# Kernel optimization log

Measured on AMD Instinct MI355X. Metric: run time of the kernel, lower is better.

Reference implementation:

```python
import math
import jax, jax.numpy as jnp
import numpy as np

N = 65536   # total nodes across episodes
H = 512     # hidden size
B = 4096    # number of episodes / decoding items
M = 32      # max neighbors (padded ragged valid_actions)


def setup_inputs() -> dict:
    key = jax.random.key(0)
    ks = jax.random.split(key, 9)
    s = 1.0 / math.sqrt(H)
    return {
        "h_static": jax.random.normal(ks[0], (N, H), jnp.float32),
        "h_dynamic": jax.random.normal(ks[1], (N, H), jnp.float32),
        "Ws_kvl": jax.random.normal(ks[2], (H, 3 * H), jnp.float32) * s,
        "Wd_kvl": jax.random.normal(ks[3], (H, 3 * H), jnp.float32) * s,
        "Wq": jax.random.normal(ks[4], (H, H), jnp.float32) * s,
        "batch": jax.random.randint(ks[5], (N,), 0, B, jnp.int32),
        "current_nodes": jax.random.randint(ks[6], (B,), 0, N),
        "neigh_idx": jax.random.randint(ks[7], (B, M), 0, N),
        "lengths": jax.random.randint(ks[8], (B,), 0, M + 1),
    }


def reference(h_static, h_dynamic, Ws_kvl, Wd_kvl, Wq, batch, current_nodes, neigh_idx, lengths):
    # precompute(): static KVL projection (full 3H GEMM then chunk, as in torch)
    kvl_s = h_static @ Ws_kvl            # [N, 3H]
    K_s = kvl_s[:, :H]
    # forward_batch(): dynamic projection
    kvl_d = h_dynamic @ Wd_kvl           # [N, 3H]
    K_d = kvl_d[:, :H]
    K = K_s + K_d                        # [N, H]  (V is computed but unused for outputs)
    q = (h_static[current_nodes] + h_dynamic[current_nodes]) @ Wq  # [B, H]

    # padded ragged neighbor attention (replaces the Python loop over B)
    Kn = K[neigh_idx]                                        # [B, M, H]
    compat = jnp.einsum('bmh,bh->bm', Kn, q) / math.sqrt(H)  # [B, M]
    mask = jnp.arange(M)[None, :] < lengths[:, None]         # [B, M]
    NEG = jnp.float32(-1e9)
    logits = jnp.where(mask, compat, NEG)

    # categorical sampling via Gumbel-max (Categorical(logits).sample())
    u = jax.random.uniform(jax.random.key(1), (B, M), jnp.float32, 1e-8, 1.0)
    g = -jnp.log(-jnp.log(u))
    idx = jnp.argmax(logits + g, axis=-1)                    # [B]

    logp = jax.nn.log_softmax(logits, axis=-1)               # [B, M]
    lp = jnp.take_along_axis(logp, idx[:, None], axis=1)[:, 0]
    actions = jnp.take_along_axis(neigh_idx, idx[:, None], axis=1)[:, 0]

    # empty neighbor list -> stay at current node, log_prob 0 (matches torch branch)
    nonempty = lengths > 0
    actions = jnp.where(nonempty, actions, current_nodes)
    lp = jnp.where(nonempty, lp, jnp.float32(0.0))
    return actions, lp
```

## Files before the change

kernel.cpp:

```cpp
#include <hip/hip_runtime.h>
#include <cstdint>
#include <cstddef>

#define HDIM 512
#define NM 32
#define NBATCH 4096
#define NNODE 65536
#define CAP 16

typedef float v4f __attribute__((ext_vector_type(4)));

__device__ __forceinline__ unsigned rotl32(unsigned x, unsigned d) {
  return (x << d) | (x >> (32u - d));
}

__device__ __forceinline__ void threefry2x32(unsigned& x0, unsigned& x1) {
  const unsigned ks0 = 0u, ks1 = 1u, ks2 = 0x1BD11BDBu;
  x0 += ks0; x1 += ks1;
#define TF_RND(r) { x0 += x1; x1 = rotl32(x1, (r)); x1 ^= x0; }
  TF_RND(13) TF_RND(15) TF_RND(26) TF_RND(6)
  x0 += ks1; x1 += ks2 + 1u;
  TF_RND(17) TF_RND(29) TF_RND(16) TF_RND(24)
  x0 += ks2; x1 += ks0 + 2u;
  TF_RND(13) TF_RND(15) TF_RND(26) TF_RND(6)
  x0 += ks0; x1 += ks1 + 3u;
  TF_RND(17) TF_RND(29) TF_RND(16) TF_RND(24)
  x0 += ks1; x1 += ks2 + 4u;
  TF_RND(13) TF_RND(15) TF_RND(26) TF_RND(6)
  x0 += ks2; x1 += ks0 + 5u;
#undef TF_RND
}

__global__ __launch_bounds__(256) void zero_cnt(int* __restrict__ cnt,
                                                int* __restrict__ ovf_cnt) {
  const int t = blockIdx.x * 256 + threadIdx.x;
  ((int4*)cnt)[t] = make_int4(0, 0, 0, 0);
  if (t == 0) *ovf_cnt = 0;
}

__global__ __launch_bounds__(256) void b1_and_index(
    const float* __restrict__ Ws, const float* __restrict__ Wd,
    const float* __restrict__ Wq, float* __restrict__ M2T,
    const int* __restrict__ neigh, const int* __restrict__ lens,
    int* __restrict__ cnt, int* __restrict__ bucket,
    int* __restrict__ ovf_cnt, int* __restrict__ ovf_list) {
  constexpr int BK = 16, LDT = 68;
  __shared__ float Ast[BK][LDT];
  __shared__ float Bst[BK][LDT];
  const int bid = blockIdx.x;
  const int tid = threadIdx.x;
  if (bid >= 128) {
    const int t = (bid - 128) * 256 + tid;
    const int b = t >> 5, m = t & 31;
    if (m < lens[b]) {
      const int n = neigh[t];
      const int slot = atomicAdd(&cnt[n], 1);
      if (slot < CAP) bucket[n * CAP + slot] = t;
      else { const int o = atomicAdd(ovf_cnt, 1); ovf_list[o] = t; }
    }
    return;
  }
  const int row0 = (bid >> 3) * 64;
  const int col0 = (bid & 7) * 64;
  const float* Abase = (row0 < 512) ? Ws : Wd;
  const int arow0 = (row0 < 512) ? row0 : row0 - 512;
  const int tx = tid & 15, ty = tid >> 4;
  const int lr = tid >> 2, lc = (tid & 3) * 4;
  float acc[4][4] = {};
  for (int k0 = 0; k0 < 512; k0 += BK) {
    float4 va = *(const float4*)(Abase + (size_t)(arow0 + lr) * 1536 + k0 + lc);
    float4 vb = *(const float4*)(Wq + (size_t)(col0 + lr) * 512 + k0 + lc);
    Ast[lc + 0][lr] = va.x; Ast[lc + 1][lr] = va.y;
    Ast[lc + 2][lr] = va.z; Ast[lc + 3][lr] = va.w;
    Bst[lc + 0][lr] = vb.x; Bst[lc + 1][lr] = vb.y;
    Bst[lc + 2][lr] = vb.z; Bst[lc + 3][lr] = vb.w;
    __syncthreads();
#pragma unroll
    for (int k = 0; k < BK; ++k) {
      float4 a4 = *(const float4*)&Ast[k][ty * 4];
      float4 b4 = *(const float4*)&Bst[k][tx * 4];
      float a[4] = {a4.x, a4.y, a4.z, a4.w};
      float bb[4] = {b4.x, b4.y, b4.z, b4.w};
#pragma unroll
      for (int i = 0; i < 4; ++i)
#pragma unroll
        for (int j = 0; j < 4; ++j) acc[i][j] += a[i] * bb[j];
    }
    __syncthreads();
  }
#pragma unroll
  for (int i = 0; i < 4; ++i) {
    float4 o;
    o.x = acc[i][0]; o.y = acc[i][1]; o.z = acc[i][2]; o.w = acc[i][3];
    *(float4*)(M2T + (size_t)(row0 + ty * 4 + i) * 512 + col0 + tx * 4) = o;
  }
}

__global__ __launch_bounds__(256) void gemm_v(const float* __restrict__ hs,
                                              const float* __restrict__ hd,
                                              const int* __restrict__ cur,
                                              const float* __restrict__ Bm,
                                              float* __restrict__ C) {
  constexpr int BK = 16, LDTA = 260, LDTB = 68;
  __shared__ float Ast[2][BK][LDTA];
  __shared__ float Bst[2][BK][LDTB];
  const int tid = threadIdx.x;
  const int swz = (blockIdx.x & 7) * 32 + (blockIdx.x >> 3);
  const int row0 = (swz >> 4) * 256;
  const int col0 = (swz & 15) * 64;
  const int tx = tid & 7, ty = tid >> 3;
  const int ar = tid >> 2;
  const int af = (tid & 3) * 4;

  size_t na[4];
#pragma unroll
  for (int q = 0; q < 4; ++q)
    na[q] = (size_t)cur[row0 + ar + 64 * q] * HDIM + af;
  const float* bp = Bm + (size_t)(col0 + ar) * 512 + af;

  float4 sa[4], sd[4], vb;
#pragma unroll
  for (int q = 0; q < 4; ++q) {
    sa[q] = *(const float4*)(hs + na[q]);
    sd[q] = *(const float4*)(hd + na[q]);
  }
  vb = *(const float4*)(bp);

  float acc[8][8] = {};
  int cb = 0;
#pragma unroll 1
  for (int t = 0; t < 32; ++t) {
#pragma unroll
    for (int q = 0; q < 4; ++q) {
      Ast[cb][af + 0][ar + 64 * q] = sa[q].x + sd[q].x;
      Ast[cb][af + 1][ar + 64 * q] = sa[q].y + sd[q].y;
      Ast[cb][af + 2][ar + 64 * q] = sa[q].z + sd[q].z;
      Ast[cb][af + 3][ar + 64 * q] = sa[q].w + sd[q].w;
    }
    Bst[cb][af + 0][ar] = vb.x;
    Bst[cb][af + 1][ar] = vb.y;
    Bst[cb][af + 2][ar] = vb.z;
    Bst[cb][af + 3][ar] = vb.w;
    __syncthreads();
    if (t < 31) {
      const int k0 = (t + 1) * BK;
#pragma unroll
      for (int q = 0; q < 4; ++q) {
        sa[q] = *(const float4*)(hs + na[q] + k0);
        sd[q] = *(const float4*)(hd + na[q] + k0);
      }
      vb = *(const float4*)(bp + k0);
    }
#pragma unroll
    for (int k = 0; k < BK; ++k) {
      const float4 a0 = *(const float4*)&Ast[cb][k][ty * 8];
      const float4 a1 = *(const float4*)&Ast[cb][k][ty * 8 + 4];
      const float4 b0 = *(const float4*)&Bst[cb][k][tx * 8];
      const float4 b1 = *(const float4*)&Bst[cb][k][tx * 8 + 4];
      const float a[8] = {a0.x, a0.y, a0.z, a0.w, a1.x, a1.y, a1.z, a1.w};
      const float bb[8] = {b0.x, b0.y, b0.z, b0.w, b1.x, b1.y, b1.z, b1.w};
#pragma unroll
      for (int i = 0; i < 8; ++i)
#pragma unroll
        for (int j = 0; j < 8; ++j) acc[i][j] += a[i] * bb[j];
    }
    cb ^= 1;
  }
#pragma unroll
  for (int i = 0; i < 8; ++i) {
    float* cp = C + (size_t)(row0 + ty * 8 + i) * 1024 + col0 + tx * 8;
    float4 o0, o1;
    o0.x = acc[i][0]; o0.y = acc[i][1]; o0.z = acc[i][2]; o0.w = acc[i][3];
    o1.x = acc[i][4]; o1.y = acc[i][5]; o1.z = acc[i][6]; o1.w = acc[i][7];
    *(float4*)cp = o0;
    *(float4*)(cp + 4) = o1;
  }
}

__global__ __launch_bounds__(256) void stream_compat(
    const float* __restrict__ hs, const float* __restrict__ hd,
    const float* __restrict__ V, const int* __restrict__ cnt,
    const int* __restrict__ bucket, const int* __restrict__ ovf_cnt,
    const int* __restrict__ ovf_list, const int* __restrict__ neigh,
    float* __restrict__ compat) {
  const int n = blockIdx.x * 4 + (threadIdx.x >> 6);
  const int lane = threadIdx.x & 63;
  const int c = cnt[n];
  if (c != 0) {
    const v4f* a4 = (const v4f*)(hs + (size_t)n * HDIM);
    const v4f* c4 = (const v4f*)(hd + (size_t)n * HDIM);
    const v4f a0 = __builtin_nontemporal_load(a4 + lane * 2);
    const v4f a1 = __builtin_nontemporal_load(a4 + lane * 2 + 1);
    const v4f b0 = __builtin_nontemporal_load(c4 + lane * 2);
    const v4f b1 = __builtin_nontemporal_load(c4 + lane * 2 + 1);
    const int cc = (c < CAP) ? c : CAP;
    for (int e = 0; e < cc; ++e) {
      const int t = bucket[n * CAP + e];
      const int b = t >> 5;
      const float4* vrow = (const float4*)(V + (size_t)b * (2 * HDIM));
      const float4 w0 = vrow[lane * 2], w1 = vrow[lane * 2 + 1];
      const float4 u0 = vrow[128 + lane * 2], u1 = vrow[128 + lane * 2 + 1];
      float acc = a0.x * w0.x + a0.y * w0.y + a0.z * w0.z + a0.w * w0.w
                + a1.x * w1.x + a1.y * w1.y + a1.z * w1.z + a1.w * w1.w
                + b0.x * u0.x + b0.y * u0.y + b0.z * u0.z + b0.w * u0.w
                + b1.x * u1.x + b1.y * u1.y + b1.z * u1.z + b1.w * u1.w;
#pragma unroll
      for (int off = 32; off >= 1; off >>= 1) acc += __shfl_xor(acc, off);
      if (lane == 0) compat[t] = acc;
    }
  }
  if (blockIdx.x < 32) {
    const int nw = *ovf_cnt;
    for (int e = blockIdx.x * 4 + (threadIdx.x >> 6); e < nw; e += 128) {
      const int t = ovf_list[e];
      const int b = t >> 5;
      const int nn = neigh[t];
      const float4* a4 = (const float4*)(hs + (size_t)nn * HDIM);
      const float4* c4 = (const float4*)(hd + (size_t)nn * HDIM);
      const float4 a0 = a4[lane * 2], a1 = a4[lane * 2 + 1];
      const float4 b0 = c4[lane * 2], b1 = c4[lane * 2 + 1];
      const float4* vrow = (const float4*)(V + (size_t)b * (2 * HDIM));
      const float4 w0 = vrow[lane * 2], w1 = vrow[lane * 2 + 1];
      const float4 u0 = vrow[128 + lane * 2], u1 = vrow[128 + lane * 2 + 1];
      float acc = a0.x * w0.x + a0.y * w0.y + a0.z * w0.z + a0.w * w0.w
                + a1.x * w1.x + a1.y * w1.y + a1.z * w1.z + a1.w * w1.w
                + b0.x * u0.x + b0.y * u0.y + b0.z * u0.z + b0.w * u0.w
                + b1.x * u1.x + b1.y * u1.y + b1.z * u1.z + b1.w * u1.w;
#pragma unroll
      for (int off = 32; off >= 1; off >>= 1) acc += __shfl_xor(acc, off);
      if (lane == 0) compat[t] = acc;
    }
  }
}

__global__ __launch_bounds__(256) void finalize_kernel(
    const float* __restrict__ compat, const int* __restrict__ neigh,
    const int* __restrict__ lengths, const int* __restrict__ cur,
    float* __restrict__ out) {
  const int b = blockIdx.x * 4 + (threadIdx.x >> 6);
  const int tid = threadIdx.x & 63;
  const int len = lengths[b];
  const bool valid = tid < NM;
  const float NEGMAX = -3.402823466e38f;
  float logit = NEGMAX;
  if (valid) {
    const float cm = compat[b * NM + tid] / 22.62741699796952f;
    logit = (tid < len) ? cm : -1e9f;
  }
  float z = NEGMAX;
  int zi = 1 << 20;
  if (valid) {
    const unsigned i_lo = (unsigned)b * 32u + (unsigned)tid;
    unsigned x0 = 0u;
    unsigned x1 = i_lo;
    threefry2x32(x0, x1);
    const unsigned bits = x0 ^ x1;
    const float fu = __uint_as_float((bits >> 9) | 0x3f800000u) - 1.0f;
    const float uu = fmaxf(1e-8f, fu + 1e-8f);
    const float g = -logf(-logf(uu));
    z = logit + g;
    zi = tid;
  }
#pragma unroll
  for (int off = 32; off >= 1; off >>= 1) {
    const float oz = __shfl_xor(z, off);
    const int oi = __shfl_xor(zi, off);
    if (oz > z || (oz == z && oi < zi)) { z = oz; zi = oi; }
  }
  float ml = logit;
#pragma unroll
  for (int off = 32; off >= 1; off >>= 1) ml = fmaxf(ml, __shfl_xor(ml, off));
  float ex = valid ? expf(logit - ml) : 0.f;
#pragma unroll
  for (int off = 32; off >= 1; off >>= 1) ex += __shfl_xor(ex, off);
  const float lsel = __shfl(logit, zi);
  if (tid == 0) {
    float lp = lsel - ml - logf(ex);
    int act = neigh[b * NM + zi];
    if (len <= 0) { act = cur[b]; lp = 0.f; }
    out[b] = (float)act;
    out[NBATCH + b] = lp;
  }
}

extern "C" void kernel_launch(void* const* d_in, const int* in_sizes, int n_in,
                              void* d_out, int out_size, void* d_ws, size_t ws_size,
                              hipStream_t stream) {
  const float* hs = (const float*)d_in[0];
  const float* hd = (const float*)d_in[1];
  const float* Ws = (const float*)d_in[2];
  const float* Wd = (const float*)d_in[3];
  const float* Wq = (const float*)d_in[4];
  const int* cur = (const int*)d_in[6];
  const int* neigh = (const int*)d_in[7];
  const int* lens = (const int*)d_in[8];
  float* out = (float*)d_out;

  char* ws = (char*)d_ws;
  size_t off = 0;
  int* cnt = (int*)(ws + off);        off += (size_t)NNODE * 4;
  int* ovf_cnt = (int*)(ws + off);    off += 256;
  int* bucket = (int*)(ws + off);     off += (size_t)NNODE * CAP * 4;
  int* ovf_list = (int*)(ws + off);   off += (size_t)NBATCH * NM * 4;
  float* compat = (float*)(ws + off); off += (size_t)NBATCH * NM * 4;
  float* M2T = (float*)(ws + off);    off += (size_t)1024 * 512 * 4;
  float* V = (float*)(ws + off);      off += (size_t)NBATCH * 2 * HDIM * 4;

  hipLaunchKernelGGL(zero_cnt, dim3(64), dim3(256), 0, stream, cnt, ovf_cnt);
  hipLaunchKernelGGL(b1_and_index, dim3(128 + NBATCH * NM / 256), dim3(256), 0, stream,
                     Ws, Wd, Wq, M2T, neigh, lens, cnt, bucket, ovf_cnt, ovf_list);
  hipLaunchKernelGGL(gemm_v, dim3(256), dim3(256), 0, stream, hs, hd, cur, M2T, V);
  hipLaunchKernelGGL(stream_compat, dim3(NNODE / 4), dim3(256), 0, stream,
                     hs, hd, V, cnt, bucket, ovf_cnt, ovf_list, neigh, compat);
  hipLaunchKernelGGL(finalize_kernel, dim3(NBATCH / 4), dim3(256), 0, stream,
                     compat, neigh, lens, cur, out);
}
```

Before: 166.1 us.

## Split-K the V GEMM across two halves and add a reduction kernel

The gathered-query GEMM that produces V is split along K into two halves, so twice as many blocks (512 instead of 256) run, each over half the reduction length. A new reduce_v kernel then sums the two partial outputs into V. The aim is better occupancy of the many compute units with only 256 blocks. In exchange it adds about 32 MB of extra partial-result traffic and one more kernel launch.

```diff
diff --git a/kernel.cpp b/kernel.cpp
--- a/kernel.cpp
+++ b/kernel.cpp
@@ -96,18 +96,20 @@
   }
 }
 
-__global__ __launch_bounds__(256) void gemm_v(const float* __restrict__ hs,
-                                              const float* __restrict__ hd,
-                                              const int* __restrict__ cur,
-                                              const float* __restrict__ Bm,
-                                              float* __restrict__ C) {
+__global__ __launch_bounds__(256) void gemm_v_split(
+    const float* __restrict__ hs, const float* __restrict__ hd,
+    const int* __restrict__ cur, const float* __restrict__ Bm,
+    float* __restrict__ P) {
   constexpr int BK = 16, LDTA = 260, LDTB = 68;
   __shared__ float Ast[2][BK][LDTA];
   __shared__ float Bst[2][BK][LDTB];
   const int tid = threadIdx.x;
-  const int swz = (blockIdx.x & 7) * 32 + (blockIdx.x >> 3);
-  const int row0 = (swz >> 4) * 256;
-  const int col0 = (swz & 15) * 64;
+  const int swz = (blockIdx.x & 7) * 64 + (blockIdx.x >> 3);
+  const int kh = swz >> 8;
+  const int rc = swz & 255;
+  const int row0 = (rc >> 4) * 256;
+  const int col0 = (rc & 15) * 64;
+  const int kbase = kh * 256;
   const int tx = tid & 7, ty = tid >> 3;
   const int ar = tid >> 2;
   const int af = (tid & 3) * 4;
@@ -115,8 +117,8 @@
   size_t na[4];
 #pragma unroll
   for (int q = 0; q < 4; ++q)
-    na[q] = (size_t)cur[row0 + ar + 64 * q] * HDIM + af;
-  const float* bp = Bm + (size_t)(col0 + ar) * 512 + af;
+    na[q] = (size_t)cur[row0 + ar + 64 * q] * HDIM + kbase + af;
+  const float* bp = Bm + (size_t)(col0 + ar) * 512 + kbase + af;
 
   float4 sa[4], sd[4], vb;
 #pragma unroll
@@ -129,7 +131,7 @@
   float acc[8][8] = {};
   int cb = 0;
 #pragma unroll 1
-  for (int t = 0; t < 32; ++t) {
+  for (int t = 0; t < 16; ++t) {
 #pragma unroll
     for (int q = 0; q < 4; ++q) {
       Ast[cb][af + 0][ar + 64 * q] = sa[q].x + sd[q].x;
@@ -142,7 +144,7 @@
     Bst[cb][af + 2][ar] = vb.z;
     Bst[cb][af + 3][ar] = vb.w;
     __syncthreads();
-    if (t < 31) {
+    if (t < 15) {
       const int k0 = (t + 1) * BK;
 #pragma unroll
       for (int q = 0; q < 4; ++q) {
@@ -166,14 +168,29 @@
     }
     cb ^= 1;
   }
+  float* Pout = P + (size_t)kh * NBATCH * 1024;
 #pragma unroll
   for (int i = 0; i < 8; ++i) {
-    float* cp = C + (size_t)(row0 + ty * 8 + i) * 1024 + col0 + tx * 8;
+    float* cp = Pout + (size_t)(row0 + ty * 8 + i) * 1024 + col0 + tx * 8;
     float4 o0, o1;
     o0.x = acc[i][0]; o0.y = acc[i][1]; o0.z = acc[i][2]; o0.w = acc[i][3];
     o1.x = acc[i][4]; o1.y = acc[i][5]; o1.z = acc[i][6]; o1.w = acc[i][7];
     *(float4*)cp = o0;
     *(float4*)(cp + 4) = o1;
+  }
+}
+
+__global__ __launch_bounds__(256) void reduce_v(const float* __restrict__ P,
+                                                float* __restrict__ V) {
+  const float4* p0 = (const float4*)P;
+  const float4* p1 = (const float4*)(P + (size_t)NBATCH * 1024);
+  float4* v4 = (float4*)V;
+  for (size_t j = (size_t)blockIdx.x * 256 + threadIdx.x; j < 1048576u;
+       j += 524288u) {
+    const float4 a = p0[j], b = p1[j];
+    float4 r;
+    r.x = a.x + b.x; r.y = a.y + b.y; r.z = a.z + b.z; r.w = a.w + b.w;
+    v4[j] = r;
   }
 }
 
@@ -304,12 +321,14 @@
   int* ovf_list = (int*)(ws + off);   off += (size_t)NBATCH * NM * 4;
   float* compat = (float*)(ws + off); off += (size_t)NBATCH * NM * 4;
   float* M2T = (float*)(ws + off);    off += (size_t)1024 * 512 * 4;
-  float* V = (float*)(ws + off);      off += (size_t)NBATCH * 2 * HDIM * 4;
+  float* V = (float*)(ws + off);      off += (size_t)NBATCH * 1024 * 4;
+  float* P = (float*)(ws + off);      off += (size_t)2 * NBATCH * 1024 * 4;
 
   hipLaunchKernelGGL(zero_cnt, dim3(64), dim3(256), 0, stream, cnt, ovf_cnt);
   hipLaunchKernelGGL(b1_and_index, dim3(128 + NBATCH * NM / 256), dim3(256), 0, stream,
                      Ws, Wd, Wq, M2T, neigh, lens, cnt, bucket, ovf_cnt, ovf_list);
-  hipLaunchKernelGGL(gemm_v, dim3(256), dim3(256), 0, stream, hs, hd, cur, M2T, V);
+  hipLaunchKernelGGL(gemm_v_split, dim3(512), dim3(256), 0, stream, hs, hd, cur, M2T, P);
+  hipLaunchKernelGGL(reduce_v, dim3(2048), dim3(256), 0, stream, P, V);
   hipLaunchKernelGGL(stream_compat, dim3(NNODE / 4), dim3(256), 0, stream,
                      hs, hd, V, cnt, bucket, ovf_cnt, ovf_list, neigh, compat);
   hipLaunchKernelGGL(finalize_kernel, dim3(NBATCH / 4), dim3(256), 0, stream,
```

Measured after the change: 179.2 us. 7.9% more time.

## Split gemm_v K dimension across two thread teams with smem reduction

Applied to the files above, without the earlier changes.

The gathered-q GEMM tile shrinks from 256x64 to 128x64 rows, doubling the grid to 512 blocks, and each block's 256 threads form two teams. Each team handles half of the K=512 reduction, and the two partial accumulators are summed through shared memory before the store. The aim is more parallelism and occupancy on a small GEMM that launched only 256 blocks. The cost is dropping register double-buffering in favour of a load, sync, store, sync loop, plus an extra reduction step and about 50KB of shared memory per block.

```diff
diff --git a/kernel.cpp b/kernel.cpp
--- a/kernel.cpp
+++ b/kernel.cpp
@@ -101,62 +101,68 @@
                                               const int* __restrict__ cur,
                                               const float* __restrict__ Bm,
                                               float* __restrict__ C) {
-  constexpr int BK = 16, LDTA = 260, LDTB = 68;
-  __shared__ float Ast[2][BK][LDTA];
-  __shared__ float Bst[2][BK][LDTB];
+  __shared__ __align__(16) char smem[51200];
+  float* As = (float*)smem;
+  float* Bs = (float*)(smem + 33792);
+  float* mg = (float*)smem;
+
   const int tid = threadIdx.x;
-  const int swz = (blockIdx.x & 7) * 32 + (blockIdx.x >> 3);
-  const int row0 = (swz >> 4) * 256;
+  const int team = tid >> 7;
+  const int lt = tid & 127;
+  const int swz = (blockIdx.x & 7) * 64 + (blockIdx.x >> 3);
+  const int row0 = (swz >> 4) * 128;
   const int col0 = (swz & 15) * 64;
-  const int tx = tid & 7, ty = tid >> 3;
-  const int ar = tid >> 2;
-  const int af = (tid & 3) * 4;
-
-  size_t na[4];
-#pragma unroll
-  for (int q = 0; q < 4; ++q)
-    na[q] = (size_t)cur[row0 + ar + 64 * q] * HDIM + af;
-  const float* bp = Bm + (size_t)(col0 + ar) * 512 + af;
-
-  float4 sa[4], sd[4], vb;
-#pragma unroll
-  for (int q = 0; q < 4; ++q) {
-    sa[q] = *(const float4*)(hs + na[q]);
-    sd[q] = *(const float4*)(hd + na[q]);
-  }
-  vb = *(const float4*)(bp);
+  const int tx = tid & 7;
+  const int ty = (tid >> 3) & 15;
+  const int r0 = lt >> 3;
+  const int cq = (lt & 7) * 4;
+  const int kb = team * 256;
+  const int aoff = team * 4224;
+  const int boff = team * 2176;
+
+  size_t na[8];
+#pragma unroll
+  for (int p = 0; p < 8; ++p)
+    na[p] = (size_t)cur[row0 + r0 + 16 * p] * HDIM + kb + cq;
+  const float* bbase = Bm + (size_t)(col0 + r0) * 512 + kb + cq;
 
   float acc[8][8] = {};
-  int cb = 0;
 #pragma unroll 1
-  for (int t = 0; t < 32; ++t) {
-#pragma unroll
-    for (int q = 0; q < 4; ++q) {
-      Ast[cb][af + 0][ar + 64 * q] = sa[q].x + sd[q].x;
-      Ast[cb][af + 1][ar + 64 * q] = sa[q].y + sd[q].y;
-      Ast[cb][af + 2][ar + 64 * q] = sa[q].z + sd[q].z;
-      Ast[cb][af + 3][ar + 64 * q] = sa[q].w + sd[q].w;
-    }
-    Bst[cb][af + 0][ar] = vb.x;
-    Bst[cb][af + 1][ar] = vb.y;
-    Bst[cb][af + 2][ar] = vb.z;
-    Bst[cb][af + 3][ar] = vb.w;
+  for (int t = 0; t < 8; ++t) {
+    const int k0 = t * 32;
+    float4 va[8], vd[8], vb[4];
+#pragma unroll
+    for (int p = 0; p < 8; ++p) {
+      va[p] = *(const float4*)(hs + na[p] + k0);
+      vd[p] = *(const float4*)(hd + na[p] + k0);
+    }
+#pragma unroll
+    for (int p = 0; p < 4; ++p)
+      vb[p] = *(const float4*)(bbase + p * (16 * 512) + k0);
     __syncthreads();
-    if (t < 31) {
-      const int k0 = (t + 1) * BK;
-#pragma unroll
-      for (int q = 0; q < 4; ++q) {
-        sa[q] = *(const float4*)(hs + na[q] + k0);
-        sd[q] = *(const float4*)(hd + na[q] + k0);
-      }
-      vb = *(const float4*)(bp + k0);
-    }
-#pragma unroll
-    for (int k = 0; k < BK; ++k) {
-      const float4 a0 = *(const float4*)&Ast[cb][k][ty * 8];
-      const float4 a1 = *(const float4*)&Ast[cb][k][ty * 8 + 4];
-      const float4 b0 = *(const float4*)&Bst[cb][k][tx * 8];
-      const float4 b1 = *(const float4*)&Bst[cb][k][tx * 8 + 4];
+#pragma unroll
+    for (int p = 0; p < 8; ++p) {
+      const int r = r0 + 16 * p;
+      As[aoff + (cq + 0) * 132 + r] = va[p].x + vd[p].x;
+      As[aoff + (cq + 1) * 132 + r] = va[p].y + vd[p].y;
+      As[aoff + (cq + 2) * 132 + r] = va[p].z + vd[p].z;
+      As[aoff + (cq + 3) * 132 + r] = va[p].w + vd[p].w;
+    }
+#pragma unroll
+    for (int p = 0; p < 4; ++p) {
+      const int r = r0 + 16 * p;
+      Bs[boff + (cq + 0) * 68 + r] = vb[p].x;
+      Bs[boff + (cq + 1) * 68 + r] = vb[p].y;
+      Bs[boff + (cq + 2) * 68 + r] = vb[p].z;
+      Bs[boff + (cq + 3) * 68 + r] = vb[p].w;
+    }
+    __syncthreads();
+#pragma unroll
+    for (int k = 0; k < 32; ++k) {
+      const float4 a0 = *(const float4*)&As[aoff + k * 132 + ty * 8];
+      const float4 a1 = *(const float4*)&As[aoff + k * 132 + ty * 8 + 4];
+      const float4 b0 = *(const float4*)&Bs[boff + k * 68 + tx * 8];
+      const float4 b1 = *(const float4*)&Bs[boff + k * 68 + tx * 8 + 4];
       const float a[8] = {a0.x, a0.y, a0.z, a0.w, a1.x, a1.y, a1.z, a1.w};
       const float bb[8] = {b0.x, b0.y, b0.z, b0.w, b1.x, b1.y, b1.z, b1.w};
 #pragma unroll
@@ -164,16 +170,29 @@
 #pragma unroll
         for (int j = 0; j < 8; ++j) acc[i][j] += a[i] * bb[j];
     }
-    cb ^= 1;
-  }
-#pragma unroll
-  for (int i = 0; i < 8; ++i) {
-    float* cp = C + (size_t)(row0 + ty * 8 + i) * 1024 + col0 + tx * 8;
-    float4 o0, o1;
-    o0.x = acc[i][0]; o0.y = acc[i][1]; o0.z = acc[i][2]; o0.w = acc[i][3];
-    o1.x = acc[i][4]; o1.y = acc[i][5]; o1.z = acc[i][6]; o1.w = acc[i][7];
-    *(float4*)cp = o0;
-    *(float4*)(cp + 4) = o1;
+  }
+  __syncthreads();
+  if (team == 1) {
+#pragma unroll
+    for (int i = 0; i < 8; ++i)
+#pragma unroll
+      for (int j = 0; j < 8; ++j)
+        mg[lt * 65 + i * 8 + j] = acc[i][j];
+  }
+  __syncthreads();
+  if (team == 0) {
+#pragma unroll
+    for (int i = 0; i < 8; ++i) {
+#pragma unroll
+      for (int j = 0; j < 8; ++j)
+        acc[i][j] = acc[i][j] + mg[lt * 65 + i * 8 + j];
+      float* cp = C + (size_t)(row0 + ty * 8 + i) * 1024 + col0 + tx * 8;
+      float4 o0, o1;
+      o0.x = acc[i][0]; o0.y = acc[i][1]; o0.z = acc[i][2]; o0.w = acc[i][3];
+      o1.x = acc[i][4]; o1.y = acc[i][5]; o1.z = acc[i][6]; o1.w = acc[i][7];
+      *(float4*)cp = o0;
+      *(float4*)(cp + 4) = o1;
+    }
   }
 }
 
@@ -304,12 +323,12 @@
   int* ovf_list = (int*)(ws + off);   off += (size_t)NBATCH * NM * 4;
   float* compat = (float*)(ws + off); off += (size_t)NBATCH * NM * 4;
   float* M2T = (float*)(ws + off);    off += (size_t)1024 * 512 * 4;
-  float* V = (float*)(ws + off);      off += (size_t)NBATCH * 2 * HDIM * 4;
+  float* V = (float*)(ws + off);      off += (size_t)NBATCH * 1024 * 4;
 
   hipLaunchKernelGGL(zero_cnt, dim3(64), dim3(256), 0, stream, cnt, ovf_cnt);
   hipLaunchKernelGGL(b1_and_index, dim3(128 + NBATCH * NM / 256), dim3(256), 0, stream,
                      Ws, Wd, Wq, M2T, neigh, lens, cnt, bucket, ovf_cnt, ovf_list);
-  hipLaunchKernelGGL(gemm_v, dim3(256), dim3(256), 0, stream, hs, hd, cur, M2T, V);
+  hipLaunchKernelGGL(gemm_v, dim3(512), dim3(256), 0, stream, hs, hd, cur, M2T, V);
   hipLaunchKernelGGL(stream_compat, dim3(NNODE / 4), dim3(256), 0, stream,
                      hs, hd, V, cnt, bucket, ovf_cnt, ovf_list, neigh, compat);
   hipLaunchKernelGGL(finalize_kernel, dim3(NBATCH / 4), dim3(256), 0, stream,
```

Result: faster. 159.5 us (-4.0%).
